# Kernel tuning notes

Hardware: AMD Instinct MI355X
Metric: run time of the kernel (lower is better)

The kernel has to match this reference:

```python
import jax, jax.numpy as jnp
import numpy as np

N, E = 50000, 800000
IN_C, HID, OUT_C = 128, 64, 40

def setup_inputs() -> dict:
    key = jax.random.key(0)
    ks = jax.random.split(key, 16)
    def w(k, shape, fan_in):
        return jax.random.normal(k, shape, dtype=jnp.float32) * (1.0 / np.sqrt(fan_in))
    x = jax.random.normal(ks[0], (N, IN_C), dtype=jnp.float32)
    edge_index = jax.random.randint(ks[1], (2, E), 0, N, dtype=jnp.int64)
    return {
        "x": x,
        "edge_index": edge_index,
        "W1": w(ks[2], (IN_C, HID), IN_C), "b1": jnp.zeros((HID,), jnp.float32),
        "W2": w(ks[3], (HID, HID), HID),   "b2": jnp.zeros((HID,), jnp.float32),
        "W3": w(ks[4], (HID, HID), HID),   "b3": jnp.zeros((HID,), jnp.float32),
        "g1": jnp.ones((HID,), jnp.float32), "be1": jnp.zeros((HID,), jnp.float32),
        "g2": jnp.ones((HID,), jnp.float32), "be2": jnp.zeros((HID,), jnp.float32),
        "M1": w(ks[5], (HID, HID), HID),   "mb1": jnp.zeros((HID,), jnp.float32),
        "M2": w(ks[6], (HID, OUT_C), HID), "mb2": jnp.zeros((OUT_C,), jnp.float32),
        "batch_size": N,
    }

def reference(x, edge_index, W1, b1, W2, b2, W3, b3, g1, be1, g2, be2, M1, mb1, M2, mb2, batch_size):
    src, dst = edge_index[0], edge_index[1]
    n = x.shape[0]
    # GCN symmetric norm with self-loops: deg over destination, +1 for self loop
    deg = jax.ops.segment_sum(jnp.ones(src.shape[0], x.dtype), dst, num_segments=n) + 1.0
    dinv = jax.lax.rsqrt(deg)  # deg >= 1 always
    enorm = (dinv[src] * dinv[dst])[:, None]  # [E,1]
    sloop = (dinv * dinv)[:, None]            # [N,1] self-loop norm

    def gcn_conv(h, W, b):
        hw = h @ W                                              # [N,H] transform first
        agg = jax.ops.segment_sum(enorm * hw[src], dst, num_segments=n)
        return agg + sloop * hw + b

    def layer_norm(h, g, be):
        mu = jnp.mean(h, axis=-1, keepdims=True)
        var = jnp.var(h, axis=-1, keepdims=True)
        return (h - mu) * jax.lax.rsqrt(var + 1e-5) * g + be

    h = jax.nn.relu(layer_norm(gcn_conv(x, W1, b1), g1, be1))
    h = jax.nn.relu(layer_norm(gcn_conv(h, W2, b2), g2, be2))
    h = gcn_conv(h, W3, b3)
    # MLP: Linear -> ReLU -> Linear
    h = jax.nn.relu(h @ M1 + mb1) @ M2 + mb2
    return jax.nn.softmax(h[:batch_size], axis=1)
```

## Files before the change

kernel.cpp:

```cpp
#include <hip/hip_runtime.h>
#include <math.h>

#define HID   64
#define OUTC  40
#define CAP   64

__global__ void zero_kernel(int4* __restrict__ p, int n4) {
    int i = blockIdx.x * blockDim.x + threadIdx.x;
    if (i < n4) p[i] = make_int4(0, 0, 0, 0);
}

__global__ void fill_kernel(const int* __restrict__ src, const int* __restrict__ dst,
                            int* __restrict__ cnt, int* __restrict__ recs,
                            int E, int N) {
    int g    = blockIdx.x & 7;
    int gblk = blockIdx.x >> 3;
    int nblk = gridDim.x >> 3;
    int slice = (N + 7) >> 3;
    int lo = g * slice;
    int hi = lo + slice; if (hi > N) hi = N;
    for (int e = gblk * blockDim.x + threadIdx.x; e < E; e += nblk * blockDim.x) {
        int d = dst[e];
        if (d >= lo && d < hi) {
            int pos = atomicAdd(&cnt[d], 1);
            if (pos < CAP) recs[(size_t)d * CAP + pos] = src[e];
        }
    }
}

__global__ void dinv_kernel(const int* __restrict__ cnt, float* __restrict__ dinv, int N) {
    int i = blockIdx.x * blockDim.x + threadIdx.x;
    if (i < N) dinv[i] = rsqrtf((float)cnt[i] + 1.0f);
}

#define FMA16(acc, a, b) \
    acc[0][0] = fmaf(a.x, b.x, acc[0][0]); acc[0][1] = fmaf(a.x, b.y, acc[0][1]); \
    acc[0][2] = fmaf(a.x, b.z, acc[0][2]); acc[0][3] = fmaf(a.x, b.w, acc[0][3]); \
    acc[1][0] = fmaf(a.y, b.x, acc[1][0]); acc[1][1] = fmaf(a.y, b.y, acc[1][1]); \
    acc[1][2] = fmaf(a.y, b.z, acc[1][2]); acc[1][3] = fmaf(a.y, b.w, acc[1][3]); \
    acc[2][0] = fmaf(a.z, b.x, acc[2][0]); acc[2][1] = fmaf(a.z, b.y, acc[2][1]); \
    acc[2][2] = fmaf(a.z, b.z, acc[2][2]); acc[2][3] = fmaf(a.z, b.w, acc[2][3]); \
    acc[3][0] = fmaf(a.w, b.x, acc[3][0]); acc[3][1] = fmaf(a.w, b.y, acc[3][1]); \
    acc[3][2] = fmaf(a.w, b.z, acc[3][2]); acc[3][3] = fmaf(a.w, b.w, acc[3][3]);

template<int CIN>
__global__ __launch_bounds__(256) void xform_kernel(const float* __restrict__ X,
                                                    const float* __restrict__ W,
                                                    float* __restrict__ out, int N) {
    __shared__ float Xs[CIN][68];
    __shared__ float Ws[CIN][68];
    int tid = threadIdx.x;
    int base = blockIdx.x << 6;
    int rows = N - base; if (rows > 64) rows = 64;

    {
        int k = tid >> 4, c = (tid & 15) << 2;
        #pragma unroll
        for (int k0 = 0; k0 < CIN; k0 += 16) {
            float4 wv = *(const float4*)(W + (size_t)((k0 + k) << 6) + c);
            *(float4*)&Ws[k0 + k][c] = wv;
        }
    }
    {
        int r = tid >> 2, q = (tid & 3) << 2;
        int rc = r < rows ? r : 0;
        const float* xp = X + (size_t)(base + rc) * CIN + q;
        #pragma unroll
        for (int k0 = 0; k0 < CIN; k0 += 16) {
            float4 xv = *(const float4*)(xp + k0);
            Xs[k0 + q + 0][r] = xv.x;
            Xs[k0 + q + 1][r] = xv.y;
            Xs[k0 + q + 2][r] = xv.z;
            Xs[k0 + q + 3][r] = xv.w;
        }
    }
    __syncthreads();

    int tx = tid & 15, ty = tid >> 4;
    float acc[4][4] = {};
    #pragma unroll 4
    for (int k = 0; k < CIN; k++) {
        float4 a = *(const float4*)&Xs[k][ty << 2];
        float4 b = *(const float4*)&Ws[k][tx << 2];
        FMA16(acc, a, b)
    }
    #pragma unroll
    for (int rr = 0; rr < 4; rr++) {
        int row = (ty << 2) + rr;
        if (row < rows)
            *(float4*)(out + ((size_t)(base + row) << 6) + (tx << 2)) =
                make_float4(acc[rr][0], acc[rr][1], acc[rr][2], acc[rr][3]);
    }
}

template<bool LN>
__global__ void conv_kernel(const float* __restrict__ hw, const int* __restrict__ recs,
                            const int* __restrict__ cnt, const float* __restrict__ dinv,
                            const float* __restrict__ b, const float* __restrict__ g,
                            const float* __restrict__ be, float* __restrict__ out, int N) {
    int lane = threadIdx.x & 63;
    int row  = (blockIdx.x << 2) + (threadIdx.x >> 6);
    if (row >= N) return;

    int c = cnt[row];
    if (c > CAP) c = CAP;

    int s_l = 0; float ds_l = 0.f;
    if (lane < c) { s_l = recs[(size_t)row * CAP + lane]; ds_l = dinv[s_l]; }

    int g4 = lane >> 4, j = lane & 15;
    const float4* hw4 = (const float4*)hw;
    float di = dinv[row];
    float4 self4 = hw4[(size_t)row * 16 + j];

    float4 a0 = {0,0,0,0}, a1 = {0,0,0,0}, a2 = {0,0,0,0}, a3 = {0,0,0,0};
    int kmax = (c + 15) & ~15;
    for (int k = 0; k < kmax; k += 16) {
        int   s0 = __shfl(s_l, k + g4 + 0), s1 = __shfl(s_l, k + g4 + 4);
        int   s2 = __shfl(s_l, k + g4 + 8), s3 = __shfl(s_l, k + g4 + 12);
        float e0 = __shfl(ds_l, k + g4 + 0), e1 = __shfl(ds_l, k + g4 + 4);
        float e2 = __shfl(ds_l, k + g4 + 8), e3 = __shfl(ds_l, k + g4 + 12);
        float4 v0 = hw4[(size_t)s0 * 16 + j];
        float4 v1 = hw4[(size_t)s1 * 16 + j];
        float4 v2 = hw4[(size_t)s2 * 16 + j];
        float4 v3 = hw4[(size_t)s3 * 16 + j];
        a0.x = fmaf(e0, v0.x, a0.x); a0.y = fmaf(e0, v0.y, a0.y);
        a0.z = fmaf(e0, v0.z, a0.z); a0.w = fmaf(e0, v0.w, a0.w);
        a1.x = fmaf(e1, v1.x, a1.x); a1.y = fmaf(e1, v1.y, a1.y);
        a1.z = fmaf(e1, v1.z, a1.z); a1.w = fmaf(e1, v1.w, a1.w);
        a2.x = fmaf(e2, v2.x, a2.x); a2.y = fmaf(e2, v2.y, a2.y);
        a2.z = fmaf(e2, v2.z, a2.z); a2.w = fmaf(e2, v2.w, a2.w);
        a3.x = fmaf(e3, v3.x, a3.x); a3.y = fmaf(e3, v3.y, a3.y);
        a3.z = fmaf(e3, v3.z, a3.z); a3.w = fmaf(e3, v3.w, a3.w);
    }
    float4 acc;
    acc.x = (a0.x + a1.x) + (a2.x + a3.x);
    acc.y = (a0.y + a1.y) + (a2.y + a3.y);
    acc.z = (a0.z + a1.z) + (a2.z + a3.z);
    acc.w = (a0.w + a1.w) + (a2.w + a3.w);
    acc.x += __shfl_xor(acc.x, 16); acc.y += __shfl_xor(acc.y, 16);
    acc.z += __shfl_xor(acc.z, 16); acc.w += __shfl_xor(acc.w, 16);
    acc.x += __shfl_xor(acc.x, 32); acc.y += __shfl_xor(acc.y, 32);
    acc.z += __shfl_xor(acc.z, 32); acc.w += __shfl_xor(acc.w, 32);

    float4 b4 = ((const float4*)b)[j];
    float dd = di * di;
    acc.x = fmaf(di, acc.x, fmaf(dd, self4.x, b4.x));
    acc.y = fmaf(di, acc.y, fmaf(dd, self4.y, b4.y));
    acc.z = fmaf(di, acc.z, fmaf(dd, self4.z, b4.z));
    acc.w = fmaf(di, acc.w, fmaf(dd, self4.w, b4.w));

    if (LN) {
        float s = (acc.x + acc.y) + (acc.z + acc.w);
        #pragma unroll
        for (int o = 8; o; o >>= 1) s += __shfl_xor(s, o);
        float mu = s * (1.f / 64.f);
        float4 d0 = make_float4(acc.x - mu, acc.y - mu, acc.z - mu, acc.w - mu);
        float v = (d0.x * d0.x + d0.y * d0.y) + (d0.z * d0.z + d0.w * d0.w);
        #pragma unroll
        for (int o = 8; o; o >>= 1) v += __shfl_xor(v, o);
        float r = rsqrtf(v * (1.f / 64.f) + 1e-5f);
        float4 g4v = ((const float4*)g)[j];
        float4 be4 = ((const float4*)be)[j];
        acc.x = fmaxf(fmaf(d0.x * r, g4v.x, be4.x), 0.f);
        acc.y = fmaxf(fmaf(d0.y * r, g4v.y, be4.y), 0.f);
        acc.z = fmaxf(fmaf(d0.z * r, g4v.z, be4.z), 0.f);
        acc.w = fmaxf(fmaf(d0.w * r, g4v.w, be4.w), 0.f);
    }
    if (g4 == 0) ((float4*)out)[(size_t)row * 16 + j] = acc;
}

__global__ __launch_bounds__(256) void mlp_kernel(const float* __restrict__ h,
                           const float* __restrict__ M1, const float* __restrict__ mb1,
                           const float* __restrict__ M2, const float* __restrict__ mb2,
                           float* __restrict__ out, int N) {
    __shared__ float Hs [64][68];
    __shared__ float W1s[64][68];
    __shared__ float H2s[64][68];
    __shared__ float W2s[64][44];
    int tid = threadIdx.x;
    int base = blockIdx.x << 6;
    int rows = N - base; if (rows > 64) rows = 64;

    {
        int k = tid >> 4, c = (tid & 15) << 2;
        #pragma unroll
        for (int k0 = 0; k0 < 64; k0 += 16) {
            float4 wv = *(const float4*)(M1 + (size_t)((k0 + k) << 6) + c);
            *(float4*)&W1s[k0 + k][c] = wv;
        }
    }
    for (int i = tid; i < 64 * OUTC; i += 256)
        W2s[i / OUTC][i % OUTC] = M2[i];
    {
        int r = tid >> 2, q = (tid & 3) << 2;
        int rc = r < rows ? r : 0;
        const float* xp = h + (((size_t)(base + rc)) << 6) + q;
        #pragma unroll
        for (int k0 = 0; k0 < 64; k0 += 16) {
            float4 xv = *(const float4*)(xp + k0);
            Hs[k0 + q + 0][r] = xv.x;
            Hs[k0 + q + 1][r] = xv.y;
            Hs[k0 + q + 2][r] = xv.z;
            Hs[k0 + q + 3][r] = xv.w;
        }
    }
    __syncthreads();

    int tx = tid & 15, ty = tid >> 4;

    float acc[4][4] = {};
    #pragma unroll 4
    for (int k = 0; k < 64; k++) {
        float4 a = *(const float4*)&Hs[k][ty << 2];
        float4 b = *(const float4*)&W1s[k][tx << 2];
        FMA16(acc, a, b)
    }
    float4 b1v = *(const float4*)(mb1 + (tx << 2));
    #pragma unroll
    for (int cc = 0; cc < 4; cc++) {
        float bc = cc == 0 ? b1v.x : cc == 1 ? b1v.y : cc == 2 ? b1v.z : b1v.w;
        #pragma unroll
        for (int rr = 0; rr < 4; rr++)
            H2s[(tx << 2) + cc][(ty << 2) + rr] = fmaxf(acc[rr][cc] + bc, 0.f);
    }
    __syncthreads();

    int bx = (tx < 10) ? (tx << 2) : 0;
    float acc2[4][4] = {};
    #pragma unroll 4
    for (int k = 0; k < 64; k++) {
        float4 a = *(const float4*)&H2s[k][ty << 2];
        float4 b = *(const float4*)&W2s[k][bx];
        FMA16(acc2, a, b)
    }
    float4 b2v = *(const float4*)(mb2 + bx);

    #pragma unroll
    for (int rr = 0; rr < 4; rr++) {
        float v0 = acc2[rr][0] + b2v.x, v1 = acc2[rr][1] + b2v.y;
        float v2 = acc2[rr][2] + b2v.z, v3 = acc2[rr][3] + b2v.w;
        float m = fmaxf(fmaxf(v0, v1), fmaxf(v2, v3));
        if (tx >= 10) m = -1e30f;
        #pragma unroll
        for (int s = 1; s < 16; s <<= 1) m = fmaxf(m, __shfl_xor(m, s));
        float e0 = __expf(v0 - m), e1 = __expf(v1 - m);
        float e2 = __expf(v2 - m), e3 = __expf(v3 - m);
        float sum = (tx < 10) ? (e0 + e1) + (e2 + e3) : 0.f;
        #pragma unroll
        for (int s = 1; s < 16; s <<= 1) sum += __shfl_xor(sum, s);
        float inv = 1.f / sum;
        int row = (ty << 2) + rr;
        if (tx < 10 && row < rows)
            *(float4*)(out + (size_t)(base + row) * OUTC + bx) =
                make_float4(e0 * inv, e1 * inv, e2 * inv, e3 * inv);
    }
}

extern "C" void kernel_launch(void* const* d_in, const int* in_sizes, int n_in,
                              void* d_out, int out_size, void* d_ws, size_t ws_size,
                              hipStream_t stream) {
    const float* x   = (const float*)d_in[0];
    const int*   ei  = (const int*)  d_in[1];
    const float* W1  = (const float*)d_in[2];
    const float* b1  = (const float*)d_in[3];
    const float* W2  = (const float*)d_in[4];
    const float* b2  = (const float*)d_in[5];
    const float* W3  = (const float*)d_in[6];
    const float* b3  = (const float*)d_in[7];
    const float* g1  = (const float*)d_in[8];
    const float* be1 = (const float*)d_in[9];
    const float* g2  = (const float*)d_in[10];
    const float* be2 = (const float*)d_in[11];
    const float* M1  = (const float*)d_in[12];
    const float* mb1 = (const float*)d_in[13];
    const float* M2  = (const float*)d_in[14];
    const float* mb2 = (const float*)d_in[15];

    const int IN_C = 128;
    int N = in_sizes[0] / IN_C;
    int E = in_sizes[1] / 2;
    const int* src = ei;
    const int* dst = ei + E;

    char* ws = (char*)d_ws;
    size_t off = 0;
    auto carve = [&](size_t bytes) -> void* {
        void* p = ws + off;
        off = (off + bytes + 255) & ~(size_t)255;
        return p;
    };
    int*   cnt  = (int*)  carve(((size_t)N + 4) * sizeof(int));
    float* dinv = (float*)carve((size_t)N * sizeof(float));
    int*   recs = (int*)  carve((size_t)N * CAP * sizeof(int));
    float* HW   = (float*)carve((size_t)N * HID * sizeof(float));
    float* H    = (float*)carve((size_t)N * HID * sizeof(float));

    int n4 = (N + 3) / 4;
    zero_kernel<<<(n4 + 255) / 256, 256, 0, stream>>>((int4*)cnt, n4);

    int nb = (N + 255) / 256;
    int rb = (N + 3) / 4;
    int tb = (N + 63) / 64;

    fill_kernel<<<2048, 256, 0, stream>>>(src, dst, cnt, recs, E, N);
    dinv_kernel<<<nb, 256, 0, stream>>>(cnt, dinv, N);

    xform_kernel<128><<<tb, 256, 0, stream>>>(x, W1, HW, N);
    conv_kernel<true><<<rb, 256, 0, stream>>>(HW, recs, cnt, dinv, b1, g1, be1, H, N);
    xform_kernel<64><<<tb, 256, 0, stream>>>(H, W2, HW, N);
    conv_kernel<true><<<rb, 256, 0, stream>>>(HW, recs, cnt, dinv, b2, g2, be2, H, N);
    xform_kernel<64><<<tb, 256, 0, stream>>>(H, W3, HW, N);
    conv_kernel<false><<<rb, 256, 0, stream>>>(HW, recs, cnt, dinv, b3, nullptr, nullptr, H, N);

    mlp_kernel<<<tb, 256, 0, stream>>>(H, M1, mb1, M2, mb2, (float*)d_out, N);
}
```

Baseline: 209.6 us.

## Store transformed features in fp16 and split conv gather by feature halves

The xform kernel now writes hw in half precision, halving the bytes gathered per neighbor in the aggregation. The conv kernel is restructured so that each block handles one 32-feature half of a row, with 16 lanes per row group. Blocks are ordered by feature half in an interleaved pattern so that each half's gather working set is more cache-friendly. LayerNorm+ReLU moves into a separate ln_kernel, which adds an extra fp32 round trip and two more launches. It also reduces accuracy from fp16 rounding of the transformed features.

```diff
diff --git a/kernel.cpp b/kernel.cpp
--- a/kernel.cpp
+++ b/kernel.cpp
@@ -1,4 +1,5 @@
 #include <hip/hip_runtime.h>
+#include <hip/hip_fp16.h>
 #include <math.h>
 
 #define HID   64
@@ -46,7 +47,7 @@
 template<int CIN>
 __global__ __launch_bounds__(256) void xform_kernel(const float* __restrict__ X,
                                                     const float* __restrict__ W,
-                                                    float* __restrict__ out, int N) {
+                                                    __half* __restrict__ out, int N) {
     __shared__ float Xs[CIN][68];
     __shared__ float Ws[CIN][68];
     int tid = threadIdx.x;
@@ -87,87 +88,104 @@
     #pragma unroll
     for (int rr = 0; rr < 4; rr++) {
         int row = (ty << 2) + rr;
-        if (row < rows)
-            *(float4*)(out + ((size_t)(base + row) << 6) + (tx << 2)) =
-                make_float4(acc[rr][0], acc[rr][1], acc[rr][2], acc[rr][3]);
-    }
-}
-
-template<bool LN>
-__global__ void conv_kernel(const float* __restrict__ hw, const int* __restrict__ recs,
-                            const int* __restrict__ cnt, const float* __restrict__ dinv,
-                            const float* __restrict__ b, const float* __restrict__ g,
-                            const float* __restrict__ be, float* __restrict__ out, int N) {
+        if (row < rows) {
+            union { uint2 u; __half2 h[2]; } pk;
+            pk.h[0] = __float22half2_rn(make_float2(acc[rr][0], acc[rr][1]));
+            pk.h[1] = __float22half2_rn(make_float2(acc[rr][2], acc[rr][3]));
+            *(uint2*)(out + ((size_t)(base + row) << 6) + (tx << 2)) = pk.u;
+        }
+    }
+}
+
+__global__ __launch_bounds__(256) void conv_kernel(
+        const __half* __restrict__ hwh, const int* __restrict__ recs,
+        const int* __restrict__ cnt, const float* __restrict__ dinv,
+        const float* __restrict__ b, float* __restrict__ out, int N) {
+    int r7 = blockIdx.x & 7;
+    int fh = r7 >> 2;
+    int nodeblk = ((blockIdx.x >> 3) << 2) + (r7 & 3);
+    int row = (nodeblk << 2) + (threadIdx.x >> 6);
+    if (row >= N) return;
     int lane = threadIdx.x & 63;
-    int row  = (blockIdx.x << 2) + (threadIdx.x >> 6);
-    if (row >= N) return;
-
-    int c = cnt[row];
-    if (c > CAP) c = CAP;
-
+    int g = lane >> 2, j = lane & 3;
+
+    int c = cnt[row]; if (c > CAP) c = CAP;
     int s_l = 0; float ds_l = 0.f;
     if (lane < c) { s_l = recs[(size_t)row * CAP + lane]; ds_l = dinv[s_l]; }
 
-    int g4 = lane >> 4, j = lane & 15;
-    const float4* hw4 = (const float4*)hw;
+    const uint4* hw16 = (const uint4*)hwh;
+    int hbase = (fh << 2) + j;
     float di = dinv[row];
-    float4 self4 = hw4[(size_t)row * 16 + j];
-
-    float4 a0 = {0,0,0,0}, a1 = {0,0,0,0}, a2 = {0,0,0,0}, a3 = {0,0,0,0};
-    int kmax = (c + 15) & ~15;
-    for (int k = 0; k < kmax; k += 16) {
-        int   s0 = __shfl(s_l, k + g4 + 0), s1 = __shfl(s_l, k + g4 + 4);
-        int   s2 = __shfl(s_l, k + g4 + 8), s3 = __shfl(s_l, k + g4 + 12);
-        float e0 = __shfl(ds_l, k + g4 + 0), e1 = __shfl(ds_l, k + g4 + 4);
-        float e2 = __shfl(ds_l, k + g4 + 8), e3 = __shfl(ds_l, k + g4 + 12);
-        float4 v0 = hw4[(size_t)s0 * 16 + j];
-        float4 v1 = hw4[(size_t)s1 * 16 + j];
-        float4 v2 = hw4[(size_t)s2 * 16 + j];
-        float4 v3 = hw4[(size_t)s3 * 16 + j];
-        a0.x = fmaf(e0, v0.x, a0.x); a0.y = fmaf(e0, v0.y, a0.y);
-        a0.z = fmaf(e0, v0.z, a0.z); a0.w = fmaf(e0, v0.w, a0.w);
-        a1.x = fmaf(e1, v1.x, a1.x); a1.y = fmaf(e1, v1.y, a1.y);
-        a1.z = fmaf(e1, v1.z, a1.z); a1.w = fmaf(e1, v1.w, a1.w);
-        a2.x = fmaf(e2, v2.x, a2.x); a2.y = fmaf(e2, v2.y, a2.y);
-        a2.z = fmaf(e2, v2.z, a2.z); a2.w = fmaf(e2, v2.w, a2.w);
-        a3.x = fmaf(e3, v3.x, a3.x); a3.y = fmaf(e3, v3.y, a3.y);
-        a3.z = fmaf(e3, v3.z, a3.z); a3.w = fmaf(e3, v3.w, a3.w);
-    }
-    float4 acc;
-    acc.x = (a0.x + a1.x) + (a2.x + a3.x);
-    acc.y = (a0.y + a1.y) + (a2.y + a3.y);
-    acc.z = (a0.z + a1.z) + (a2.z + a3.z);
-    acc.w = (a0.w + a1.w) + (a2.w + a3.w);
-    acc.x += __shfl_xor(acc.x, 16); acc.y += __shfl_xor(acc.y, 16);
-    acc.z += __shfl_xor(acc.z, 16); acc.w += __shfl_xor(acc.w, 16);
-    acc.x += __shfl_xor(acc.x, 32); acc.y += __shfl_xor(acc.y, 32);
-    acc.z += __shfl_xor(acc.z, 32); acc.w += __shfl_xor(acc.w, 32);
-
-    float4 b4 = ((const float4*)b)[j];
-    float dd = di * di;
-    acc.x = fmaf(di, acc.x, fmaf(dd, self4.x, b4.x));
-    acc.y = fmaf(di, acc.y, fmaf(dd, self4.y, b4.y));
-    acc.z = fmaf(di, acc.z, fmaf(dd, self4.z, b4.z));
-    acc.w = fmaf(di, acc.w, fmaf(dd, self4.w, b4.w));
-
-    if (LN) {
-        float s = (acc.x + acc.y) + (acc.z + acc.w);
-        #pragma unroll
-        for (int o = 8; o; o >>= 1) s += __shfl_xor(s, o);
-        float mu = s * (1.f / 64.f);
-        float4 d0 = make_float4(acc.x - mu, acc.y - mu, acc.z - mu, acc.w - mu);
-        float v = (d0.x * d0.x + d0.y * d0.y) + (d0.z * d0.z + d0.w * d0.w);
-        #pragma unroll
-        for (int o = 8; o; o >>= 1) v += __shfl_xor(v, o);
-        float r = rsqrtf(v * (1.f / 64.f) + 1e-5f);
-        float4 g4v = ((const float4*)g)[j];
-        float4 be4 = ((const float4*)be)[j];
-        acc.x = fmaxf(fmaf(d0.x * r, g4v.x, be4.x), 0.f);
-        acc.y = fmaxf(fmaf(d0.y * r, g4v.y, be4.y), 0.f);
-        acc.z = fmaxf(fmaf(d0.z * r, g4v.z, be4.z), 0.f);
-        acc.w = fmaxf(fmaf(d0.w * r, g4v.w, be4.w), 0.f);
-    }
-    if (g4 == 0) ((float4*)out)[(size_t)row * 16 + j] = acc;
+    uint4 selfv = hw16[(size_t)row * 8 + hbase];
+
+    float acc[8] = {0,0,0,0,0,0,0,0};
+    int kmax = (c + 31) & ~31;
+    for (int k = 0; k < kmax; k += 32) {
+        int   s0 = __shfl(s_l, k + g),  s1 = __shfl(s_l, k + 16 + g);
+        float e0 = __shfl(ds_l, k + g), e1 = __shfl(ds_l, k + 16 + g);
+        uint4 v0 = hw16[(size_t)s0 * 8 + hbase];
+        uint4 v1 = hw16[(size_t)s1 * 8 + hbase];
+        const __half2* h0 = (const __half2*)&v0;
+        const __half2* h1 = (const __half2*)&v1;
+        #pragma unroll
+        for (int t = 0; t < 4; t++) {
+            float2 f0 = __half22float2(h0[t]);
+            float2 f1 = __half22float2(h1[t]);
+            acc[2*t]   = fmaf(e0, f0.x, acc[2*t]);
+            acc[2*t+1] = fmaf(e0, f0.y, acc[2*t+1]);
+            acc[2*t]   = fmaf(e1, f1.x, acc[2*t]);
+            acc[2*t+1] = fmaf(e1, f1.y, acc[2*t+1]);
+        }
+    }
+    #pragma unroll
+    for (int off = 4; off < 64; off <<= 1) {
+        #pragma unroll
+        for (int t = 0; t < 8; t++) acc[t] += __shfl_xor(acc[t], off);
+    }
+    if (g == 0) {
+        int f0 = (fh << 5) + (j << 3);
+        const __half2* sp = (const __half2*)&selfv;
+        float dd = di * di;
+        float bb[8], res[8];
+        *(float4*)&bb[0] = *(const float4*)(b + f0);
+        *(float4*)&bb[4] = *(const float4*)(b + f0 + 4);
+        #pragma unroll
+        for (int t = 0; t < 4; t++) {
+            float2 f = __half22float2(sp[t]);
+            res[2*t]   = fmaf(di, acc[2*t],   fmaf(dd, f.x, bb[2*t]));
+            res[2*t+1] = fmaf(di, acc[2*t+1], fmaf(dd, f.y, bb[2*t+1]));
+        }
+        *(float4*)(out + (size_t)row * 64 + f0)     = *(float4*)&res[0];
+        *(float4*)(out + (size_t)row * 64 + f0 + 4) = *(float4*)&res[4];
+    }
+}
+
+__global__ __launch_bounds__(256) void ln_kernel(const float* __restrict__ ph,
+                                                 const float* __restrict__ g,
+                                                 const float* __restrict__ be,
+                                                 float* __restrict__ out, int N) {
+    int lane = threadIdx.x & 63;
+    int sub = lane >> 4, j = lane & 15;
+    int row = (blockIdx.x << 4) + ((threadIdx.x >> 6) << 2) + sub;
+    if (row >= N) return;
+    float4 v = *(const float4*)(ph + (size_t)row * 64 + (j << 2));
+    float s = (v.x + v.y) + (v.z + v.w);
+    #pragma unroll
+    for (int o = 1; o < 16; o <<= 1) s += __shfl_xor(s, o);
+    float mu = s * (1.f / 64.f);
+    float4 d = make_float4(v.x - mu, v.y - mu, v.z - mu, v.w - mu);
+    float vv = (d.x * d.x + d.y * d.y) + (d.z * d.z + d.w * d.w);
+    #pragma unroll
+    for (int o = 1; o < 16; o <<= 1) vv += __shfl_xor(vv, o);
+    float r = rsqrtf(vv * (1.f / 64.f) + 1e-5f);
+    float4 gv = *(const float4*)(g + (j << 2));
+    float4 bv = *(const float4*)(be + (j << 2));
+    float4 o4;
+    o4.x = fmaxf(fmaf(d.x * r, gv.x, bv.x), 0.f);
+    o4.y = fmaxf(fmaf(d.y * r, gv.y, bv.y), 0.f);
+    o4.z = fmaxf(fmaf(d.z * r, gv.z, bv.z), 0.f);
+    o4.w = fmaxf(fmaf(d.w * r, gv.w, bv.w), 0.f);
+    *(float4*)(out + (size_t)row * 64 + (j << 2)) = o4;
 }
 
 __global__ __launch_bounds__(256) void mlp_kernel(const float* __restrict__ h,
@@ -290,28 +308,34 @@
         off = (off + bytes + 255) & ~(size_t)255;
         return p;
     };
-    int*   cnt  = (int*)  carve(((size_t)N + 4) * sizeof(int));
-    float* dinv = (float*)carve((size_t)N * sizeof(float));
-    int*   recs = (int*)  carve((size_t)N * CAP * sizeof(int));
-    float* HW   = (float*)carve((size_t)N * HID * sizeof(float));
-    float* H    = (float*)carve((size_t)N * HID * sizeof(float));
+    int*    cnt  = (int*)   carve(((size_t)N + 4) * sizeof(int));
+    float*  dinv = (float*) carve((size_t)N * sizeof(float));
+    int*    recs = (int*)   carve((size_t)N * CAP * sizeof(int));
+    __half* HWh  = (__half*)carve((size_t)N * HID * sizeof(__half));
+    float*  PH   = (float*) carve((size_t)N * HID * sizeof(float));
+    float*  H    = (float*) carve((size_t)N * HID * sizeof(float));
 
     int n4 = (N + 3) / 4;
     zero_kernel<<<(n4 + 255) / 256, 256, 0, stream>>>((int4*)cnt, n4);
 
     int nb = (N + 255) / 256;
-    int rb = (N + 3) / 4;
     int tb = (N + 63) / 64;
+    int lb = (N + 15) / 16;
+    int nodeblks = (N + 3) / 4;
+    int nb4 = (nodeblks + 3) & ~3;
+    int cb = nb4 * 2;
 
     fill_kernel<<<2048, 256, 0, stream>>>(src, dst, cnt, recs, E, N);
     dinv_kernel<<<nb, 256, 0, stream>>>(cnt, dinv, N);
 
-    xform_kernel<128><<<tb, 256, 0, stream>>>(x, W1, HW, N);
-    conv_kernel<true><<<rb, 256, 0, stream>>>(HW, recs, cnt, dinv, b1, g1, be1, H, N);
-    xform_kernel<64><<<tb, 256, 0, stream>>>(H, W2, HW, N);
-    conv_kernel<true><<<rb, 256, 0, stream>>>(HW, recs, cnt, dinv, b2, g2, be2, H, N);
-    xform_kernel<64><<<tb, 256, 0, stream>>>(H, W3, HW, N);
-    conv_kernel<false><<<rb, 256, 0, stream>>>(HW, recs, cnt, dinv, b3, nullptr, nullptr, H, N);
-
-    mlp_kernel<<<tb, 256, 0, stream>>>(H, M1, mb1, M2, mb2, (float*)d_out, N);
-}
+    xform_kernel<128><<<tb, 256, 0, stream>>>(x, W1, HWh, N);
+    conv_kernel<<<cb, 256, 0, stream>>>(HWh, recs, cnt, dinv, b1, PH, N);
+    ln_kernel<<<lb, 256, 0, stream>>>(PH, g1, be1, H, N);
+    xform_kernel<64><<<tb, 256, 0, stream>>>(H, W2, HWh, N);
+    conv_kernel<<<cb, 256, 0, stream>>>(HWh, recs, cnt, dinv, b2, PH, N);
+    ln_kernel<<<lb, 256, 0, stream>>>(PH, g2, be2, H, N);
+    xform_kernel<64><<<tb, 256, 0, stream>>>(H, W3, HWh, N);
+    conv_kernel<<<cb, 256, 0, stream>>>(HWh, recs, cnt, dinv, b3, PH, N);
+
+    mlp_kernel<<<tb, 256, 0, stream>>>(PH, M1, mb1, M2, mb2, (float*)d_out, N);
+}
```

Measured after the change: 246.4 us. 17.6% more time.
